# Kernel optimization log

Measured on AMD Instinct MI355X. Metric: run time of the kernel, lower is better.

Reference implementation:

```python
import jax, jax.numpy as jnp
import numpy as np

NUM_HEADS = 20
MAX_SEQLEN = 1500  # max per-segment length (Whisper 30s -> 1500 frames); static for jit
NEG = -1e30


def setup_inputs() -> dict:
    key = jax.random.key(0)
    ks = jax.random.split(key, 6)
    B, S, D = 4, MAX_SEQLEN, 1280
    T = B * S
    hidden_states = jax.random.normal(ks[0], (T, D), dtype=jnp.float32)
    # packed varlen layout: 4 equal-length audio segments
    cu_seqlens = (jnp.arange(B + 1, dtype=jnp.int32) * S)
    w = 0.02
    Wq = jax.random.normal(ks[1], (D, D), dtype=jnp.float32) * w
    Wk = jax.random.normal(ks[2], (D, D), dtype=jnp.float32) * w
    Wv = jax.random.normal(ks[3], (D, D), dtype=jnp.float32) * w
    Wo = jax.random.normal(ks[4], (D, D), dtype=jnp.float32) * w
    bq = jnp.zeros((D,), jnp.float32)
    bv = jnp.zeros((D,), jnp.float32)
    bo = jnp.zeros((D,), jnp.float32)
    return {"hidden_states": hidden_states, "cu_seqlens": cu_seqlens,
            "Wq": Wq, "bq": bq, "Wk": Wk, "Wv": Wv, "bv": bv, "Wo": Wo, "bo": bo}


def _varlen_attention(hidden_states, cu_seqlens, Wq, bq, Wk, Wv, bv, Wo, bo):
    T, D = hidden_states.shape
    H = NUM_HEADS
    d = D // H
    scale = d ** -0.5
    S = MAX_SEQLEN
    B = cu_seqlens.shape[0] - 1

    # projections (torch nn.Linear convention: y = x @ W.T + b; k_proj has no bias)
    q = hidden_states @ Wq.T + bq   # [T, D]
    k = hidden_states @ Wk.T        # [T, D]
    v = hidden_states @ Wv.T + bv   # [T, D]

    lens = cu_seqlens[1:] - cu_seqlens[:-1]                 # [B]
    pos = jnp.arange(S, dtype=jnp.int32)                    # [S]
    valid = pos[None, :] < lens[:, None]                    # [B, S]
    idx = cu_seqlens[:-1, None] + pos[None, :]              # [B, S]
    idx_g = jnp.where(valid, idx, 0)

    # unpack to padded [B, S, H, d]
    qb = q[idx_g].reshape(B, S, H, d)
    kb = k[idx_g].reshape(B, S, H, d)
    vb = v[idx_g].reshape(B, S, H, d)

    scores = jnp.einsum('bqhd,bkhd->bhqk', qb, kb) * scale  # [B, H, S, S]
    scores = jnp.where(valid[:, None, None, :], scores, NEG)
    attn = jax.nn.softmax(scores, axis=-1)
    out = jnp.einsum('bhqk,bkhd->bqhd', attn, vb).reshape(B, S, D)

    # repack to [T, D]; invalid slots scatter out-of-bounds and are dropped
    idx_s = jnp.where(valid, idx, T).reshape(-1)
    packed = jnp.zeros((T, D), out.dtype).at[idx_s].set(out.reshape(-1, D), mode='drop')
    return packed @ Wo.T + bo


def reference(hidden_states, cu_seqlens, Wq, bq, Wk, Wv, bv, Wo, bo):
    return _varlen_attention(hidden_states, cu_seqlens, Wq, bq, Wk, Wv, bv, Wo, bo)
```

## Files before the change

### kernel.cpp

```cpp
#include <hip/hip_runtime.h>
#include <stdint.h>
#include <math.h>

#define DMODEL 1280
#define NHEAD  20
#define DHEAD  64
#define NSEG   4
#define MAXS   1500
#define SPAD   1536
#define TPAD   (NSEG*SPAD)
#define QT128  ((MAXS + 127) / 128)
#define BM 128
#define BN 128
#define BK 32
#define QSCALE 0.18033688011112042f
#define NEGV  -1e30f

typedef float  f32x4  __attribute__((ext_vector_type(4)));
typedef __bf16 bf16x8 __attribute__((ext_vector_type(8)));

__device__ __forceinline__ ushort f2bf(float f) {
  union { float f; uint32_t u; } a; a.f = f;
  uint32_t u = a.u;
  u += 0x7FFFu + ((u >> 16) & 1u);
  return (ushort)(u >> 16);
}

__device__ __forceinline__ uint32_t pk2(float a, float b) {
  union { float f; uint32_t u; } ua, ub; ua.f = a; ub.f = b;
  uint32_t x = ua.u + 0x8000u, y = ub.u + 0x8000u;
  return (x >> 16) | (y & 0xFFFF0000u);
}

__device__ __forceinline__ void async16(const void* g, void* lds) {
  __builtin_amdgcn_global_load_lds((const __attribute__((address_space(1))) void*)g,
                                   (__attribute__((address_space(3))) void*)lds,
                                   16, 0, 0);
}

__device__ __forceinline__ int perm32(int a) {
  return ((a >> 2) & 3) * 8 + ((a >> 4) & 1) * 4 + (a & 3);
}

__global__ void __launch_bounds__(256)
cvt_all(const float* __restrict__ hs, const float* __restrict__ Wq,
        const float* __restrict__ Wk, const float* __restrict__ Wv,
        const float* __restrict__ Wo, ushort* __restrict__ dst, int nX, int DD) {
  const int i = (blockIdx.x * 256 + threadIdx.x) * 4;
  const float* src;
  if (i < nX) {
    src = hs + i;
  } else {
    int j = i - nX;
    const int z = (j >= DD) + (j >= 2 * DD) + (j >= 3 * DD);
    const float* w = (z == 0) ? Wq : (z == 1) ? Wk : (z == 2) ? Wv : Wo;
    src = w + (j - z * DD);
  }
  float4 v = *(const float4*)src;
  ushort4 o;
  o.x = f2bf(v.x); o.y = f2bf(v.y); o.z = f2bf(v.z); o.w = f2bf(v.w);
  *(ushort4*)(dst + i) = o;
}

__device__ __forceinline__ void gemm_tile_mainloop(
    const ushort* __restrict__ A, const ushort* __restrict__ W,
    int M, int m0, int n0, ushort* As, ushort* Bs, f32x4 (&acc)[4][4])
{
  const int tid  = threadIdx.x;
  const int wave = tid >> 6, lane = tid & 63;
  const int quad = lane >> 4, c16 = lane & 15;
  const int wr = (wave >> 1) * 64, wc = (wave & 1) * 64;

  const int M0 = wave * 128 + lane, M1 = M0 + 64;
  const int sr0 = M0 >> 3, pp0 = M0 & 7, p0 = pp0 ^ (sr0 & 7);
  const int sr1 = M1 >> 3, pp1 = M1 & 7, p1 = pp1 ^ (sr1 & 7);
  const int row0 = sr0 * 2 + (p0 >> 2), kc0 = (p0 & 3) << 3;
  const int row1 = sr1 * 2 + (p1 >> 2), kc1 = (p1 & 3) << 3;
  int ga0 = m0 + row0; if (ga0 > M - 1) ga0 = M - 1;
  int ga1 = m0 + row1; if (ga1 > M - 1) ga1 = M - 1;
  const ushort* Ap0 = A + (size_t)ga0 * DMODEL + kc0;
  const ushort* Ap1 = A + (size_t)ga1 * DMODEL + kc1;
  const ushort* Bp0 = W + (size_t)(n0 + row0) * DMODEL + kc0;
  const ushort* Bp1 = W + (size_t)(n0 + row1) * DMODEL + kc1;
  const int o0 = wave * 1024;
  const int o1 = wave * 1024 + 512;
  const int BUF = BM * BK;

  async16(Ap0, As + o0); async16(Ap1, As + o1);
  async16(Bp0, Bs + o0); async16(Bp1, Bs + o1);

  int c = 0;
  for (int k0 = 0; k0 < DMODEL; k0 += BK, c ^= 1) {
    __syncthreads();
    if (k0 + BK < DMODEL) {
      const int kn = k0 + BK;
      const int bo = (c ^ 1) * BUF;
      async16(Ap0 + kn, As + bo + o0); async16(Ap1 + kn, As + bo + o1);
      async16(Bp0 + kn, Bs + bo + o0); async16(Bp1 + kn, Bs + bo + o1);
    }
    const ushort* Ab = As + c * BUF;
    const ushort* Bb = Bs + c * BUF;
    bf16x8 a[4], b[4];
#pragma unroll
    for (int i = 0; i < 4; ++i) {
      const int row = wr + i * 16 + c16;
      const int sr = row >> 1;
      const int off = (sr << 6) + (((((row & 1) << 2) | quad) ^ (sr & 7)) << 3);
      a[i] = *(const bf16x8*)(Ab + off);
    }
#pragma unroll
    for (int j = 0; j < 4; ++j) {
      const int row = wc + j * 16 + c16;
      const int sr = row >> 1;
      const int off = (sr << 6) + (((((row & 1) << 2) | quad) ^ (sr & 7)) << 3);
      b[j] = *(const bf16x8*)(Bb + off);
    }
#pragma unroll
    for (int i = 0; i < 4; ++i)
#pragma unroll
      for (int j = 0; j < 4; ++j)
        acc[i][j] = __builtin_amdgcn_mfma_f32_16x16x32_bf16(a[i], b[j], acc[i][j], 0, 0, 0);
  }
}

__global__ void __launch_bounds__(256, 3)
gemm_qkv(const ushort* __restrict__ X, const ushort* __restrict__ W4,
         const float* __restrict__ bq, const float* __restrict__ bv,
         const int* __restrict__ cu,
         ushort* __restrict__ qb, ushort* __restrict__ kb, ushort* __restrict__ vt, int M)
{
  __shared__ ushort As[2 * BM * BK], Bs[2 * BN * BK];
  const int wg = blockIdx.x;
  if (wg >= 30) return;
  const int z = wg / 10;
  const int n0 = (wg % 10) * BN;
  const int m0 = blockIdx.y * BM;
  const ushort* W = W4 + (size_t)z * DMODEL * DMODEL;

  f32x4 acc[4][4];
  f32x4 zero = {0.f, 0.f, 0.f, 0.f};
#pragma unroll
  for (int i = 0; i < 4; ++i)
#pragma unroll
    for (int j = 0; j < 4; ++j) acc[i][j] = zero;

  gemm_tile_mainloop(X, W, M, m0, n0, As, Bs, acc);

  const int tid = threadIdx.x, wave = tid >> 6, lane = tid & 63;
  const int quad = lane >> 4, c16 = lane & 15;
  const int wr = (wave >> 1) * 64, wc = (wave & 1) * 64;

  if (z == 2) {
    const int c1 = cu[1], c2 = cu[2], c3 = cu[3];
#pragma unroll
    for (int i = 0; i < 4; ++i) {
      const int t0 = m0 + wr + i * 16 + quad * 4;
      const int s0a = (t0 >= c1) + (t0 >= c2) + (t0 >= c3);
      const int s3a = (t0 + 3 >= c1) + (t0 + 3 >= c2) + (t0 + 3 >= c3);
      const int seg0 = (s0a == 0) ? 0 : (s0a == 1) ? c1 : (s0a == 2) ? c2 : c3;
#pragma unroll
      for (int j = 0; j < 4; ++j) {
        const int cfeat = n0 + wc + j * 16 + c16;
        const float bb = bv[cfeat];
        if (t0 + 3 < M && s0a == s3a) {
          const int s = t0 - seg0;
          const size_t base = (size_t)cfeat * TPAD + (size_t)s0a * SPAD
                            + (size_t)(s & ~31) + perm32(s & 31);
          ushort4 w;
          w.x = f2bf(acc[i][j][0] + bb);
          w.y = f2bf(acc[i][j][1] + bb);
          w.z = f2bf(acc[i][j][2] + bb);
          w.w = f2bf(acc[i][j][3] + bb);
          *(ushort4*)(vt + base) = w;
        } else {
#pragma unroll
          for (int r = 0; r < 4; ++r) {
            const int t = t0 + r;
            if (t < M) {
              const int sb = (t >= c1) + (t >= c2) + (t >= c3);
              const int sg = (sb == 0) ? 0 : (sb == 1) ? c1 : (sb == 2) ? c2 : c3;
              const int s = t - sg;
              vt[(size_t)cfeat * TPAD + (size_t)sb * SPAD + (s & ~31) + perm32(s & 31)]
                  = f2bf(acc[i][j][r] + bb);
            }
          }
        }
      }
    }
  } else {
    ushort* out = (z == 0) ? qb : kb;
    const float* bias = (z == 0) ? bq : (const float*)nullptr;
    const float oscale = (z == 0) ? QSCALE : 1.0f;
#pragma unroll
    for (int i = 0; i < 4; ++i) {
      const int rbase = m0 + wr + i * 16 + quad * 4;
#pragma unroll
      for (int j = 0; j < 4; ++j) {
        const int c = n0 + wc + j * 16 + c16;
        const float bb = bias ? bias[c] : 0.f;
#pragma unroll
        for (int r = 0; r < 4; ++r) {
          const int rr = rbase + r;
          if (rr < M) out[(size_t)rr * DMODEL + c] = f2bf((acc[i][j][r] + bb) * oscale);
        }
      }
    }
  }
}

__global__ void __launch_bounds__(256, 3)
gemm_out(const ushort* __restrict__ A, const ushort* __restrict__ W,
         const float* __restrict__ bias, float* __restrict__ out, int M)
{
  __shared__ ushort As[2 * BM * BK], Bs[2 * BN * BK];
  const int wg = blockIdx.x;
  if (wg >= 10) return;
  const int n0 = wg * BN;
  const int m0 = blockIdx.y * BM;
  f32x4 acc[4][4];
  f32x4 zero = {0.f, 0.f, 0.f, 0.f};
#pragma unroll
  for (int i = 0; i < 4; ++i)
#pragma unroll
    for (int j = 0; j < 4; ++j) acc[i][j] = zero;

  gemm_tile_mainloop(A, W, M, m0, n0, As, Bs, acc);

  const int tid = threadIdx.x, wave = tid >> 6, lane = tid & 63;
  const int quad = lane >> 4, c16 = lane & 15;
  const int wr = (wave >> 1) * 64, wc = (wave & 1) * 64;
#pragma unroll
  for (int i = 0; i < 4; ++i) {
    const int rbase = m0 + wr + i * 16 + quad * 4;
#pragma unroll
    for (int j = 0; j < 4; ++j) {
      const int c = n0 + wc + j * 16 + c16;
      const float bb = bias[c];
#pragma unroll
      for (int r = 0; r < 4; ++r) {
        const int rr = rbase + r;
        if (rr < M) out[(size_t)rr * DMODEL + c] = acc[i][j][r] + bb;
      }
    }
  }
}

__global__ void __launch_bounds__(256, 3)
attn_fused(const ushort* __restrict__ qb, const ushort* __restrict__ kb,
           const ushort* __restrict__ vt, ushort* __restrict__ ob,
           const int* __restrict__ cu, int T)
{
  __shared__ ushort Qs[128 * 64];
  __shared__ ushort Ks[2][64 * 64];
  __shared__ ushort Vs[2][64 * 64];
  const int hs = blockIdx.x;
  const int b = hs / NHEAD, h = hs % NHEAD;
  const int seg0 = cu[b];
  const int len  = cu[b + 1] - seg0;
  const int q0 = blockIdx.y * 128;
  if (q0 >= len) return;
  const int tid = threadIdx.x, wave = tid >> 6, lane = tid & 63;
  const int quad = lane >> 4, c16 = lane & 15;

#pragma unroll
  for (int t = 0; t < 4; ++t) {
    const int M = t * 256 + wave * 64 + lane;
    const int r = M >> 3, k2 = M & 7;
    const int col = ((k2 ^ (r & 7)) << 3);
    int qr = q0 + r; if (qr >= len) qr = len - 1;
    async16(qb + (size_t)(seg0 + qr) * DMODEL + h * DHEAD + col,
            Qs + (t * 256 + wave * 64) * 8);
  }

  const int niter = (len + 63) >> 6;
#pragma unroll
  for (int t = 0; t < 2; ++t) {
    const int M = t * 256 + wave * 64 + lane;
    const int r = M >> 3, k2 = M & 7;
    const int col = ((k2 ^ (r & 7)) << 3);
    int rr = r; if (rr > len - 1) rr = len - 1;
    async16(kb + (size_t)(seg0 + rr) * DMODEL + h * DHEAD + col,
            Ks[0] + (t * 256 + wave * 64) * 8);
    async16(vt + (size_t)(h * DHEAD + r) * TPAD + (size_t)b * SPAD + col,
            Vs[0] + (t * 256 + wave * 64) * 8);
  }

  bf16x8 aq[2][2];
  float l_i[2] = {0.f, 0.f};
  f32x4 o_acc[2][4];
  f32x4 zero = {0.f, 0.f, 0.f, 0.f};
#pragma unroll
  for (int n = 0; n < 2; ++n)
#pragma unroll
    for (int m = 0; m < 4; ++m) o_acc[n][m] = zero;

  for (int it = 0; it < niter; ++it) {
    const int kv0 = it * 64;
    const int c = it & 1;
    __syncthreads();

    if (it + 1 < niter) {
      const int kvn = kv0 + 64;
      const int lim = len - 1 - kvn;
#pragma unroll
      for (int t = 0; t < 2; ++t) {
        const int M = t * 256 + wave * 64 + lane;
        const int r = M >> 3, k2 = M & 7;
        const int col = ((k2 ^ (r & 7)) << 3);
        int rr = r; if (rr > lim) rr = lim;
        async16(kb + (size_t)(seg0 + kvn + rr) * DMODEL + h * DHEAD + col,
                Ks[c ^ 1] + (t * 256 + wave * 64) * 8);
        async16(vt + (size_t)(h * DHEAD + r) * TPAD + (size_t)b * SPAD + kvn + col,
                Vs[c ^ 1] + (t * 256 + wave * 64) * 8);
      }
    }

    if (it == 0) {
#pragma unroll
      for (int n = 0; n < 2; ++n)
#pragma unroll
        for (int ks = 0; ks < 2; ++ks) {
          const int row = wave * 32 + n * 16 + c16;
          aq[n][ks] = *(const bf16x8*)(Qs + row * 64 + (((ks * 4 + quad) ^ (c16 & 7)) << 3));
        }
    }

    f32x4 s[2][4];
#pragma unroll
    for (int f = 0; f < 4; ++f) {
      const int row = f * 16 + c16;
      const int ch = c16 & 7;
      bf16x8 ak0 = *(const bf16x8*)(Ks[c] + row * 64 + ((quad ^ ch) << 3));
      bf16x8 ak1 = *(const bf16x8*)(Ks[c] + row * 64 + (((4 + quad) ^ ch) << 3));
#pragma unroll
      for (int n = 0; n < 2; ++n) {
        s[n][f] = zero;
        s[n][f] = __builtin_amdgcn_mfma_f32_16x16x32_bf16(ak0, aq[n][0], s[n][f], 0, 0, 0);
        s[n][f] = __builtin_amdgcn_mfma_f32_16x16x32_bf16(ak1, aq[n][1], s[n][f], 0, 0, 0);
      }
    }

    if (kv0 + 64 > len) {
#pragma unroll
      for (int f = 0; f < 4; ++f) {
        const int kvb = kv0 + f * 16 + quad * 4;
#pragma unroll
        for (int r = 0; r < 4; ++r)
          if (kvb + r >= len) { s[0][f][r] = NEGV; s[1][f][r] = NEGV; }
      }
    }

#pragma unroll
    for (int n = 0; n < 2; ++n) {
      float rs = 0.f;
#pragma unroll
      for (int f = 0; f < 4; ++f)
#pragma unroll
        for (int r = 0; r < 4; ++r) {
          const float p = exp2f(s[n][f][r]);
          s[n][f][r] = p;
          rs += p;
        }
      l_i[n] += rs;
    }

    bf16x8 bp[2][2];
#pragma unroll
    for (int n = 0; n < 2; ++n)
#pragma unroll
      for (int g = 0; g < 2; ++g) {
        union { uint32_t u[4]; bf16x8 v; } cv;
        cv.u[0] = pk2(s[n][2 * g][0], s[n][2 * g][1]);
        cv.u[1] = pk2(s[n][2 * g][2], s[n][2 * g][3]);
        cv.u[2] = pk2(s[n][2 * g + 1][0], s[n][2 * g + 1][1]);
        cv.u[3] = pk2(s[n][2 * g + 1][2], s[n][2 * g + 1][3]);
        bp[n][g] = cv.v;
      }

#pragma unroll
    for (int m = 0; m < 4; ++m) {
      const int row = m * 16 + c16;
      const int ch = c16 & 7;
      bf16x8 av0 = *(const bf16x8*)(Vs[c] + row * 64 + ((quad ^ ch) << 3));
      bf16x8 av1 = *(const bf16x8*)(Vs[c] + row * 64 + (((4 + quad) ^ ch) << 3));
#pragma unroll
      for (int n = 0; n < 2; ++n) {
        o_acc[n][m] = __builtin_amdgcn_mfma_f32_16x16x32_bf16(av0, bp[n][0], o_acc[n][m], 0, 0, 0);
        o_acc[n][m] = __builtin_amdgcn_mfma_f32_16x16x32_bf16(av1, bp[n][1], o_acc[n][m], 0, 0, 0);
      }
    }
  }

#pragma unroll
  for (int n = 0; n < 2; ++n) {
    float l = l_i[n];
    l += __shfl_xor(l, 16);
    l += __shfl_xor(l, 32);
    const int q = q0 + wave * 32 + n * 16 + c16;
    if (q < len) {
      const float inv = 1.0f / l;
      const size_t base = (size_t)(seg0 + q) * DMODEL + h * DHEAD;
#pragma unroll
      for (int m = 0; m < 4; ++m) {
        ushort4 pk;
        pk.x = f2bf(o_acc[n][m][0] * inv);
        pk.y = f2bf(o_acc[n][m][1] * inv);
        pk.z = f2bf(o_acc[n][m][2] * inv);
        pk.w = f2bf(o_acc[n][m][3] * inv);
        *(ushort4*)(ob + base + m * 16 + quad * 4) = pk;
      }
    }
  }
}

extern "C" void kernel_launch(void* const* d_in, const int* in_sizes, int n_in,
                              void* d_out, int out_size, void* d_ws, size_t ws_size,
                              hipStream_t stream)
{
  (void)n_in; (void)out_size; (void)ws_size;
  const float* hs = (const float*)d_in[0];
  const int*   cu = (const int*)d_in[1];
  const float* Wq = (const float*)d_in[2];
  const float* bq = (const float*)d_in[3];
  const float* Wk = (const float*)d_in[4];
  const float* Wv = (const float*)d_in[5];
  const float* bv = (const float*)d_in[6];
  const float* Wo = (const float*)d_in[7];
  const float* bo = (const float*)d_in[8];
  float* out = (float*)d_out;
  const int T  = in_sizes[0] / DMODEL;
  const int DD = DMODEL * DMODEL;
  const int nX = T * DMODEL;

  ushort* ws  = (ushort*)d_ws;
  ushort* X   = ws;
  ushort* W4  = X + (size_t)nX;
  ushort* qb  = W4 + 4 * (size_t)DD;
  ushort* kb  = qb + (size_t)T * DMODEL;
  ushort* vt  = kb + (size_t)T * DMODEL;
  ushort* ob  = X;

  const int ncvt = nX + 4 * DD;
  cvt_all<<<(ncvt / 4 + 255) / 256, 256, 0, stream>>>(hs, Wq, Wk, Wv, Wo, ws, nX, DD);

  gemm_qkv<<<dim3(32, (T + BM - 1) / BM), 256, 0, stream>>>(
      X, W4, bq, bv, cu, qb, kb, vt, T);

  attn_fused<<<dim3(NSEG * NHEAD, QT128), 256, 0, stream>>>(qb, kb, vt, ob, cu, T);

  gemm_out<<<dim3(16, (T + BM - 1) / BM), 256, 0, stream>>>(
      ob, W4 + 3 * (size_t)DD, bo, out, T);
}
```

Measured before the change: 338.5 us.

## Shrink attention LDS footprint, drop bounds clamps, raise occupancy, use native exp2

The attention kernel now reuses the Q staging buffer as one half of the K/V double buffer, so shared memory drops from 48KB to 32KB per block. It also precomputes K/V pointers that advance each iteration, and loads Q fragments into registers before the loop. Row clamping is removed from the GEMM A loads and from the Q/K loads, which relies on padded buffers so out-of-range reads are safe. Launch bounds go from 3 to 4 blocks per CU, and exp2f is swapped for the AMDGCN exp2 builtin. The intent is higher occupancy and less address arithmetic, at the cost of register pressure and possible reads past the end of unpadded buffers.

Result: faster. 307.2 us (-9.3%).

```diff
diff --git a/kernel.cpp b/kernel.cpp
--- a/kernel.cpp
+++ b/kernel.cpp
@@ -19,6 +19,12 @@
 typedef float  f32x4  __attribute__((ext_vector_type(4)));
 typedef __bf16 bf16x8 __attribute__((ext_vector_type(8)));
 
+#if __has_builtin(__builtin_amdgcn_exp2f)
+#define EXP2F(x) __builtin_amdgcn_exp2f(x)
+#else
+#define EXP2F(x) exp2f(x)
+#endif
+
 __device__ __forceinline__ ushort f2bf(float f) {
   union { float f; uint32_t u; } a; a.f = f;
   uint32_t u = a.u;
@@ -76,10 +82,8 @@
   const int sr1 = M1 >> 3, pp1 = M1 & 7, p1 = pp1 ^ (sr1 & 7);
   const int row0 = sr0 * 2 + (p0 >> 2), kc0 = (p0 & 3) << 3;
   const int row1 = sr1 * 2 + (p1 >> 2), kc1 = (p1 & 3) << 3;
-  int ga0 = m0 + row0; if (ga0 > M - 1) ga0 = M - 1;
-  int ga1 = m0 + row1; if (ga1 > M - 1) ga1 = M - 1;
-  const ushort* Ap0 = A + (size_t)ga0 * DMODEL + kc0;
-  const ushort* Ap1 = A + (size_t)ga1 * DMODEL + kc1;
+  const ushort* Ap0 = A + (size_t)(m0 + row0) * DMODEL + kc0;
+  const ushort* Ap1 = A + (size_t)(m0 + row1) * DMODEL + kc1;
   const ushort* Bp0 = W + (size_t)(n0 + row0) * DMODEL + kc0;
   const ushort* Bp1 = W + (size_t)(n0 + row1) * DMODEL + kc1;
   const int o0 = wave * 1024;
@@ -123,7 +127,7 @@
   }
 }
 
-__global__ void __launch_bounds__(256, 3)
+__global__ void __launch_bounds__(256, 4)
 gemm_qkv(const ushort* __restrict__ X, const ushort* __restrict__ W4,
          const float* __restrict__ bq, const float* __restrict__ bv,
          const int* __restrict__ cu,
@@ -208,7 +212,7 @@
   }
 }
 
-__global__ void __launch_bounds__(256, 3)
+__global__ void __launch_bounds__(256, 4)
 gemm_out(const ushort* __restrict__ A, const ushort* __restrict__ W,
          const float* __restrict__ bias, float* __restrict__ out, int M)
 {
@@ -245,14 +249,12 @@
   }
 }
 
-__global__ void __launch_bounds__(256, 3)
+__global__ void __launch_bounds__(256, 4)
 attn_fused(const ushort* __restrict__ qb, const ushort* __restrict__ kb,
            const ushort* __restrict__ vt, ushort* __restrict__ ob,
            const int* __restrict__ cu, int T)
 {
-  __shared__ ushort Qs[128 * 64];
-  __shared__ ushort Ks[2][64 * 64];
-  __shared__ ushort Vs[2][64 * 64];
+  __shared__ ushort SB[2][8192];
   const int hs = blockIdx.x;
   const int b = hs / NHEAD, h = hs % NHEAD;
   const int seg0 = cu[b];
@@ -262,30 +264,43 @@
   const int tid = threadIdx.x, wave = tid >> 6, lane = tid & 63;
   const int quad = lane >> 4, c16 = lane & 15;
 
-#pragma unroll
-  for (int t = 0; t < 4; ++t) {
-    const int M = t * 256 + wave * 64 + lane;
-    const int r = M >> 3, k2 = M & 7;
-    const int col = ((k2 ^ (r & 7)) << 3);
-    int qr = q0 + r; if (qr >= len) qr = len - 1;
-    async16(qb + (size_t)(seg0 + qr) * DMODEL + h * DHEAD + col,
-            Qs + (t * 256 + wave * 64) * 8);
-  }
-
-  const int niter = (len + 63) >> 6;
-#pragma unroll
-  for (int t = 0; t < 2; ++t) {
-    const int M = t * 256 + wave * 64 + lane;
-    const int r = M >> 3, k2 = M & 7;
-    const int col = ((k2 ^ (r & 7)) << 3);
-    int rr = r; if (rr > len - 1) rr = len - 1;
-    async16(kb + (size_t)(seg0 + rr) * DMODEL + h * DHEAD + col,
-            Ks[0] + (t * 256 + wave * 64) * 8);
-    async16(vt + (size_t)(h * DHEAD + r) * TPAD + (size_t)b * SPAD + col,
-            Vs[0] + (t * 256 + wave * 64) * 8);
-  }
+  {
+    const int s = wave * 64 + lane;
+#pragma unroll
+    for (int t = 0; t < 4; ++t) {
+      const int slot = t * 256 + s;
+      const int r = slot >> 3, k2 = slot & 7;
+      const int col = ((k2 ^ (r & 7)) << 3);
+      async16(qb + (size_t)(seg0 + q0 + r) * DMODEL + h * DHEAD + col,
+              &SB[0][(t * 256 + wave * 64) * 8]);
+    }
+  }
+
+  const int sl  = wave * 64 + lane;
+  const int rr0 = sl >> 3, kk2 = sl & 7;
+  const int colc = ((kk2 ^ (rr0 & 7)) << 3);
+  const ushort* kp0 = kb + (size_t)(seg0 + rr0) * DMODEL + h * DHEAD + colc;
+  const ushort* kp1 = kp0 + (size_t)32 * DMODEL;
+  const ushort* vp0 = vt + (size_t)(h * DHEAD + rr0) * TPAD + (size_t)b * SPAD + colc;
+  const ushort* vp1 = vp0 + (size_t)32 * TPAD;
+  const int ldo0 = wave * 512;
+  const int ldo1 = 2048 + wave * 512;
+
+  __syncthreads();
 
   bf16x8 aq[2][2];
+#pragma unroll
+  for (int n = 0; n < 2; ++n)
+#pragma unroll
+    for (int ks = 0; ks < 2; ++ks) {
+      const int row = wave * 32 + n * 16 + c16;
+      aq[n][ks] = *(const bf16x8*)(&SB[0][row * 64 + (((ks * 4 + quad) ^ (c16 & 7)) << 3)]);
+    }
+
+  async16(kp0, &SB[1][ldo0]);        async16(kp1, &SB[1][ldo1]);
+  async16(vp0, &SB[1][4096 + ldo0]); async16(vp1, &SB[1][4096 + ldo1]);
+  kp0 += (size_t)64 * DMODEL; kp1 += (size_t)64 * DMODEL; vp0 += 64; vp1 += 64;
+
   float l_i[2] = {0.f, 0.f};
   f32x4 o_acc[2][4];
   f32x4 zero = {0.f, 0.f, 0.f, 0.f};
@@ -294,35 +309,17 @@
 #pragma unroll
     for (int m = 0; m < 4; ++m) o_acc[n][m] = zero;
 
+  const int niter = (len + 63) >> 6;
   for (int it = 0; it < niter; ++it) {
-    const int kv0 = it * 64;
-    const int c = it & 1;
     __syncthreads();
+    const ushort* Kt = &SB[1 ^ (it & 1)][0];
+    const ushort* Vt = &SB[1 ^ (it & 1)][4096];
 
     if (it + 1 < niter) {
-      const int kvn = kv0 + 64;
-      const int lim = len - 1 - kvn;
-#pragma unroll
-      for (int t = 0; t < 2; ++t) {
-        const int M = t * 256 + wave * 64 + lane;
-        const int r = M >> 3, k2 = M & 7;
-        const int col = ((k2 ^ (r & 7)) << 3);
-        int rr = r; if (rr > lim) rr = lim;
-        async16(kb + (size_t)(seg0 + kvn + rr) * DMODEL + h * DHEAD + col,
-                Ks[c ^ 1] + (t * 256 + wave * 64) * 8);
-        async16(vt + (size_t)(h * DHEAD + r) * TPAD + (size_t)b * SPAD + kvn + col,
-                Vs[c ^ 1] + (t * 256 + wave * 64) * 8);
-      }
-    }
-
-    if (it == 0) {
-#pragma unroll
-      for (int n = 0; n < 2; ++n)
-#pragma unroll
-        for (int ks = 0; ks < 2; ++ks) {
-          const int row = wave * 32 + n * 16 + c16;
-          aq[n][ks] = *(const bf16x8*)(Qs + row * 64 + (((ks * 4 + quad) ^ (c16 & 7)) << 3));
-        }
+      ushort* Dst = &SB[it & 1][0];
+      async16(kp0, Dst + ldo0);        async16(kp1, Dst + ldo1);
+      async16(vp0, Dst + 4096 + ldo0); async16(vp1, Dst + 4096 + ldo1);
+      kp0 += (size_t)64 * DMODEL; kp1 += (size_t)64 * DMODEL; vp0 += 64; vp1 += 64;
     }
 
     f32x4 s[2][4];
@@ -330,8 +327,8 @@
     for (int f = 0; f < 4; ++f) {
       const int row = f * 16 + c16;
       const int ch = c16 & 7;
-      bf16x8 ak0 = *(const bf16x8*)(Ks[c] + row * 64 + ((quad ^ ch) << 3));
-      bf16x8 ak1 = *(const bf16x8*)(Ks[c] + row * 64 + (((4 + quad) ^ ch) << 3));
+      bf16x8 ak0 = *(const bf16x8*)(Kt + row * 64 + ((quad ^ ch) << 3));
+      bf16x8 ak1 = *(const bf16x8*)(Kt + row * 64 + (((4 + quad) ^ ch) << 3));
 #pragma unroll
       for (int n = 0; n < 2; ++n) {
         s[n][f] = zero;
@@ -340,6 +337,7 @@
       }
     }
 
+    const int kv0 = it * 64;
     if (kv0 + 64 > len) {
 #pragma unroll
       for (int f = 0; f < 4; ++f) {
@@ -357,7 +355,7 @@
       for (int f = 0; f < 4; ++f)
 #pragma unroll
         for (int r = 0; r < 4; ++r) {
-          const float p = exp2f(s[n][f][r]);
+          const float p = EXP2F(s[n][f][r]);
           s[n][f][r] = p;
           rs += p;
         }
@@ -381,8 +379,8 @@
     for (int m = 0; m < 4; ++m) {
       const int row = m * 16 + c16;
       const int ch = c16 & 7;
-      bf16x8 av0 = *(const bf16x8*)(Vs[c] + row * 64 + ((quad ^ ch) << 3));
-      bf16x8 av1 = *(const bf16x8*)(Vs[c] + row * 64 + (((4 + quad) ^ ch) << 3));
+      bf16x8 av0 = *(const bf16x8*)(Vt + row * 64 + ((quad ^ ch) << 3));
+      bf16x8 av1 = *(const bf16x8*)(Vt + row * 64 + (((4 + quad) ^ ch) << 3));
 #pragma unroll
       for (int n = 0; n < 2; ++n) {
         o_acc[n][m] = __builtin_amdgcn_mfma_f32_16x16x32_bf16(av0, bp[n][0], o_acc[n][m], 0, 0, 0);
```
